# Kernel tuning notes

Measured on AMD Instinct MI355X. Metric: run time of the kernel, lower is better.

## Reference

```python
import jax, jax.numpy as jnp
import numpy as np

C = 17
BETA = 0.95
ALPHA = 5.0
WPC = 3.0  # weight_per_class
IGNORE = 255


def setup_inputs() -> dict:
    key = jax.random.key(0)
    k1, k2 = jax.random.split(key)
    pred = jax.random.normal(k1, (2, C, 200, 200, 16), dtype=jnp.float32)
    ssc_target = jax.random.randint(k2, (2, 200, 200, 16), 0, C, dtype=jnp.int64)
    f1_list = jnp.zeros((C,), dtype=jnp.float32)  # running F1 buffer
    return {"pred": pred, "ssc_target": ssc_target, "f1_list": f1_list}


def _bce_ones(x):
    # F.binary_cross_entropy(x, ones) = -log(x), with torch's log clamp at -100
    return jnp.minimum(-jnp.log(jnp.maximum(x, 1e-38)), 100.0)


def _sem_scal_loss(pred, ssc_target, f1_list):
    B = pred.shape[0]
    ps = jax.nn.softmax(pred, axis=1)                      # [B,C,X,Y,Z]
    mask = (ssc_target != IGNORE)                          # [B,X,Y,Z]
    mf = mask.astype(ps.dtype)
    tgt = jnp.where(mask, ssc_target, 0)                   # safe class index

    # prob of the target class at each voxel -> per-class nominator via segment_sum
    p_at = jnp.take_along_axis(ps, tgt[:, None], axis=1)[:, 0]          # [B,X,Y,Z]
    tgt_flat = tgt.reshape(-1)
    mflat = mf.reshape(-1)
    nominator = jax.ops.segment_sum(p_at.reshape(-1) * mflat, tgt_flat, num_segments=C)
    sum_comp = jax.ops.segment_sum(mflat, tgt_flat, num_segments=C)     # |{target==i}| in mask
    sum_p = jnp.einsum('bcn,bn->c', ps.reshape(B, C, -1), mf.reshape(B, -1))
    n_mask = jnp.sum(mflat)

    has = sum_comp > 0
    precision = jnp.where(sum_p > 0, nominator / jnp.where(sum_p > 0, sum_p, 1.0), 0.0)
    recall = jnp.where(has, nominator / jnp.where(has, sum_comp, 1.0), 0.0)
    neg_comp = n_mask - sum_comp                           # sum(1 - completion_target)
    spec_num = (n_mask - sum_p) - (sum_comp - nominator)   # sum((1-p)*(1-comp))
    specificity = jnp.where(neg_comp > 0, spec_num / jnp.where(neg_comp > 0, neg_comp, 1.0), 0.0)

    loss_list = jnp.where(
        has,
        jnp.where(sum_p > 0, _bce_ones(precision), 0.0)
        + _bce_ones(recall)
        + jnp.where(neg_comp > 0, _bce_ones(specificity), 0.0),
        0.0,
    )

    denom = precision + recall
    f1 = jnp.where(denom > 0, 2.0 * precision * recall / jnp.where(denom > 0, denom, 1.0), 0.0)
    cur_f1 = jnp.where(has, f1, 0.0)
    new_f1 = BETA * f1_list + (1.0 - BETA) * cur_f1        # updated running buffer

    count = jnp.sum(has.astype(ps.dtype))
    weight_pool = WPC * count

    sel = loss_list != 0
    logits = jnp.where(sel, ALPHA * (1.0 - new_f1), -jnp.inf)
    sm = jax.nn.softmax(logits)                            # softmax over selected classes
    weighted = loss_list * (1.0 + weight_pool * sm)
    loss = jnp.sum(weighted) / (count * (1.0 + WPC))
    return loss


def reference(pred, ssc_target, f1_list):
    return _sem_scal_loss(pred, ssc_target, f1_list)
```

## Files before the change

kernel.cpp:

```cpp
#include <hip/hip_runtime.h>
#include <math.h>

#define NC 17
#define PLANE 640000
#define H2 (PLANE / 2)
#define J 5
#define BPB 250
#define NBLK1 (2 * BPB)
#define PCOLS 504
#define BETA_C 0.95f
#define ALPHA_C 5.0f
#define WPC_C 3.0f
#define IGNORE_C 255

#define DPP_ADD(v, ctrl)                                                        \
    do {                                                                        \
        int _t = __builtin_amdgcn_update_dpp(0, __float_as_int(v), (ctrl),      \
                                             0xf, 0xf, true);                   \
        (v) += __int_as_float(_t);                                              \
    } while (0)

__device__ __forceinline__ float wave_sum_dpp(float v) {
    DPP_ADD(v, 0x111);
    DPP_ADD(v, 0x112);
    DPP_ADD(v, 0x114);
    DPP_ADD(v, 0x118);
    DPP_ADD(v, 0x142);
    DPP_ADD(v, 0x143);
    return v;
}


__global__ __launch_bounds__(256) void al_reduce1(const float* __restrict__ pred,
                                                  const int* __restrict__ tgt,
                                                  float* __restrict__ part) {
    const int bb  = blockIdx.x;
    const int b   = (bb >= BPB) ? 1 : 0;
    const int base = (bb - b * BPB) * (256 * J);
    const int tid = (int)threadIdx.x;
    const float2* p0 = reinterpret_cast<const float2*>(pred) + (size_t)(b * NC) * H2;
    const int2*   tg = reinterpret_cast<const int2*>(tgt) + (size_t)b * H2;

    __shared__ float lds[3 * NC];
    if (tid < 3 * NC) lds[tid] = 0.f;

    float sump[NC];
#pragma unroll
    for (int c = 0; c < NC; ++c) sump[c] = 0.f;

    float2 xA[NC], xB[NC];
    int2 tA, tB;

#define LOAD_SLAB(X, T, s)                                                      \
    do {                                                                        \
        const int n2 = base + (s) * 256 + tid;                                  \
        _Pragma("unroll")                                                       \
        for (int c = 0; c < NC; ++c) X[c] = p0[(size_t)c * H2 + n2];            \
        T = tg[n2];                                                             \
    } while (0)

#define COMP_SLAB(X, T)                                                         \
    do {                                                                        \
        float2 ss = make_float2(0.f, 0.f);                                      \
        _Pragma("unroll")                                                       \
        for (int c = 0; c < NC; ++c) {                                          \
            X[c].x = __expf(X[c].x); ss.x += X[c].x;                            \
            X[c].y = __expf(X[c].y); ss.y += X[c].y;                            \
        }                                                                       \
        const float j0 = (T.x != IGNORE_C) ? __builtin_amdgcn_rcpf(ss.x) : 0.f; \
        const float j1 = (T.y != IGNORE_C) ? __builtin_amdgcn_rcpf(ss.y) : 0.f; \
        float e0 = 0.f, e1 = 0.f;                                               \
        _Pragma("unroll")                                                       \
        for (int c = 0; c < NC; ++c) {                                          \
            sump[c] += X[c].x * j0 + X[c].y * j1;                               \
            e0 = (c == T.x) ? X[c].x : e0;                                      \
            e1 = (c == T.y) ? X[c].y : e1;                                      \
        }                                                                       \
        if (T.x != IGNORE_C) { atomicAdd(&lds[T.x], e0 * j0);                   \
                               atomicAdd(&lds[2 * NC + T.x], 1.0f); }           \
        if (T.y != IGNORE_C) { atomicAdd(&lds[T.y], e1 * j1);                   \
                               atomicAdd(&lds[2 * NC + T.y], 1.0f); }           \
    } while (0)

    LOAD_SLAB(xA, tA, 0);
    LOAD_SLAB(xB, tB, 1);
    __syncthreads();

    COMP_SLAB(xA, tA);
    LOAD_SLAB(xA, tA, 2);
    COMP_SLAB(xB, tB);
    LOAD_SLAB(xB, tB, 3);
    COMP_SLAB(xA, tA);
    LOAD_SLAB(xA, tA, 4);
    COMP_SLAB(xB, tB);
    COMP_SLAB(xA, tA);

#undef LOAD_SLAB
#undef COMP_SLAB

#pragma unroll
    for (int c = 0; c < NC; ++c) sump[c] = wave_sum_dpp(sump[c]);
    if ((tid & 63) == 63) {
#pragma unroll
        for (int c = 0; c < NC; ++c) atomicAdd(&lds[NC + c], sump[c]);
    }
    __syncthreads();

    if (tid < 3 * NC)
        part[(size_t)tid * PCOLS + bb] = lds[tid];
}

__global__ __launch_bounds__(256) void al_reduce2(const float* __restrict__ part,
                                                  float* __restrict__ acc) {
    const int r = blockIdx.x;
    const int tid = (int)threadIdx.x;
    const float* p = part + (size_t)r * PCOLS;

    float s = 0.f;
#pragma unroll
    for (int k = 0; k < 2; ++k) {
        const int i = tid + k * 256;
        s += (i < NBLK1) ? p[i] : 0.f;
    }
    s = wave_sum_dpp(s);

    __shared__ float w[4];
    if ((tid & 63) == 63) w[tid >> 6] = s;
    __syncthreads();
    if (tid == 0) acc[r] = (w[0] + w[1]) + (w[2] + w[3]);
}

__device__ __forceinline__ float bce_ones(float x) {
    return fminf(-logf(fmaxf(x, 1e-38f)), 100.0f);
}

__global__ void al_finalize(const float* __restrict__ acc,
                            const float* __restrict__ f1_list,
                            float* __restrict__ out) {
    if (threadIdx.x != 0 || blockIdx.x != 0) return;

    float nom[NC], sump[NC], cnt[NC];
    float n_mask = 0.f;
    for (int c = 0; c < NC; ++c) {
        nom[c]  = acc[c];
        sump[c] = acc[NC + c];
        cnt[c]  = acc[2 * NC + c];
        n_mask += cnt[c];
    }

    float loss_list[NC], newf1[NC];
    float count = 0.f;
    for (int c = 0; c < NC; ++c) {
        const bool has = cnt[c] > 0.f;
        const float prec = (sump[c] > 0.f) ? nom[c] / sump[c] : 0.f;
        const float rec  = has ? nom[c] / cnt[c] : 0.f;
        const float negc = n_mask - cnt[c];
        const float spec_num = (n_mask - sump[c]) - (cnt[c] - nom[c]);
        const float spec = (negc > 0.f) ? spec_num / negc : 0.f;

        float ll = 0.f;
        if (has) {
            ll  = (sump[c] > 0.f) ? bce_ones(prec) : 0.f;
            ll += bce_ones(rec);
            ll += (negc > 0.f) ? bce_ones(spec) : 0.f;
        }
        loss_list[c] = ll;

        const float den = prec + rec;
        const float f1  = (den > 0.f) ? 2.f * prec * rec / den : 0.f;
        const float cur = has ? f1 : 0.f;
        newf1[c] = BETA_C * f1_list[c] + (1.f - BETA_C) * cur;
        count += has ? 1.f : 0.f;
    }

    const float wp = WPC_C * count;

    float mxl = -INFINITY;
    for (int c = 0; c < NC; ++c) {
        const float lg = (loss_list[c] != 0.f) ? ALPHA_C * (1.f - newf1[c]) : -INFINITY;
        mxl = fmaxf(mxl, lg);
    }
    float e[NC];
    float se = 0.f;
    for (int c = 0; c < NC; ++c) {
        const float lg = (loss_list[c] != 0.f) ? ALPHA_C * (1.f - newf1[c]) : -INFINITY;
        e[c] = expf(lg - mxl);
        se += e[c];
    }

    float total = 0.f;
    for (int c = 0; c < NC; ++c) {
        const float sm = e[c] / se;
        total += loss_list[c] * (1.f + wp * sm);
    }
    out[0] = total / (count * (1.f + WPC_C));
}

extern "C" void kernel_launch(void* const* d_in, const int* in_sizes, int n_in,
                              void* d_out, int out_size, void* d_ws, size_t ws_size,
                              hipStream_t stream) {
    const float* pred    = (const float*)d_in[0];
    const int*   tgt     = (const int*)d_in[1];
    const float* f1_list = (const float*)d_in[2];
    float* out  = (float*)d_out;
    float* part = (float*)d_ws;
    float* acc  = part + (size_t)(3 * NC) * PCOLS;

    al_reduce1<<<dim3(NBLK1), dim3(256), 0, stream>>>(pred, tgt, part);
    al_reduce2<<<dim3(3 * NC), dim3(256), 0, stream>>>(part, acc);
    al_finalize<<<dim3(1), dim3(64), 0, stream>>>(acc, f1_list, out);
}
```

Measured before the change: 36.01 us.

## Fuse reduction and finalize into one kernel with last-block-done pattern

Replaces the three-kernel pipeline (per-block partial write, cross-block reduce, single-thread finalize) with one kernel. Each block atomically adds its per-class sums into padded global accumulators, and the last block to increment a done counter computes the final loss. This removes two kernel launches and the partials buffer, at the cost of a memset, global float atomics, and reliance on ordering between other waves' atomics and the counter increment (there is no block barrier before the counter). Summation order also becomes nondeterministic.

Measured after the change: 46.64 us. 29.5% more time.

```diff
diff --git a/kernel.cpp b/kernel.cpp
--- a/kernel.cpp
+++ b/kernel.cpp
@@ -7,7 +7,8 @@
 #define J 5
 #define BPB 250
 #define NBLK1 (2 * BPB)
-#define PCOLS 504
+#define SLOT 16
+#define DONE_IDX (3 * NC * SLOT)
 #define BETA_C 0.95f
 #define ALPHA_C 5.0f
 #define WPC_C 3.0f
@@ -30,10 +31,17 @@
     return v;
 }
 
+__device__ __forceinline__ float bce_ones(float x) {
+    return fminf(-logf(fmaxf(x, 1e-38f)), 100.0f);
+}
 
-__global__ __launch_bounds__(256) void al_reduce1(const float* __restrict__ pred,
-                                                  const int* __restrict__ tgt,
-                                                  float* __restrict__ part) {
+
+__global__ __launch_bounds__(256) void al_fused(const float* __restrict__ pred,
+                                                const int* __restrict__ tgt,
+                                                const float* __restrict__ f1_list,
+                                                float* __restrict__ acc,
+                                                unsigned* __restrict__ done,
+                                                float* __restrict__ out) {
     const int bb  = blockIdx.x;
     const int b   = (bb >= BPB) ? 1 : 0;
     const int base = (bb - b * BPB) * (256 * J);
@@ -106,45 +114,21 @@
     }
     __syncthreads();
 
-    if (tid < 3 * NC)
-        part[(size_t)tid * PCOLS + bb] = lds[tid];
-}
+    if (tid < 3 * NC) atomicAdd(&acc[tid * SLOT], lds[tid]);
 
-__global__ __launch_bounds__(256) void al_reduce2(const float* __restrict__ part,
-                                                  float* __restrict__ acc) {
-    const int r = blockIdx.x;
-    const int tid = (int)threadIdx.x;
-    const float* p = part + (size_t)r * PCOLS;
+    if (tid != 0) return;
 
-    float s = 0.f;
+    asm volatile("s_waitcnt vmcnt(0)" ::: "memory");
+    const unsigned old = atomicAdd(done, 1u);
+    if (old != (unsigned)(NBLK1 - 1)) return;
+
+    float nom[NC], sump2[NC], cnt[NC];
+    float n_mask = 0.f;
 #pragma unroll
-    for (int k = 0; k < 2; ++k) {
-        const int i = tid + k * 256;
-        s += (i < NBLK1) ? p[i] : 0.f;
-    }
-    s = wave_sum_dpp(s);
-
-    __shared__ float w[4];
-    if ((tid & 63) == 63) w[tid >> 6] = s;
-    __syncthreads();
-    if (tid == 0) acc[r] = (w[0] + w[1]) + (w[2] + w[3]);
-}
-
-__device__ __forceinline__ float bce_ones(float x) {
-    return fminf(-logf(fmaxf(x, 1e-38f)), 100.0f);
-}
-
-__global__ void al_finalize(const float* __restrict__ acc,
-                            const float* __restrict__ f1_list,
-                            float* __restrict__ out) {
-    if (threadIdx.x != 0 || blockIdx.x != 0) return;
-
-    float nom[NC], sump[NC], cnt[NC];
-    float n_mask = 0.f;
     for (int c = 0; c < NC; ++c) {
-        nom[c]  = acc[c];
-        sump[c] = acc[NC + c];
-        cnt[c]  = acc[2 * NC + c];
+        nom[c]   = __hip_atomic_load(&acc[c * SLOT],            __ATOMIC_RELAXED, __HIP_MEMORY_SCOPE_AGENT);
+        sump2[c] = __hip_atomic_load(&acc[(NC + c) * SLOT],     __ATOMIC_RELAXED, __HIP_MEMORY_SCOPE_AGENT);
+        cnt[c]   = __hip_atomic_load(&acc[(2 * NC + c) * SLOT], __ATOMIC_RELAXED, __HIP_MEMORY_SCOPE_AGENT);
         n_mask += cnt[c];
     }
 
@@ -152,15 +136,15 @@
     float count = 0.f;
     for (int c = 0; c < NC; ++c) {
         const bool has = cnt[c] > 0.f;
-        const float prec = (sump[c] > 0.f) ? nom[c] / sump[c] : 0.f;
+        const float prec = (sump2[c] > 0.f) ? nom[c] / sump2[c] : 0.f;
         const float rec  = has ? nom[c] / cnt[c] : 0.f;
         const float negc = n_mask - cnt[c];
-        const float spec_num = (n_mask - sump[c]) - (cnt[c] - nom[c]);
+        const float spec_num = (n_mask - sump2[c]) - (cnt[c] - nom[c]);
         const float spec = (negc > 0.f) ? spec_num / negc : 0.f;
 
         float ll = 0.f;
         if (has) {
-            ll  = (sump[c] > 0.f) ? bce_ones(prec) : 0.f;
+            ll  = (sump2[c] > 0.f) ? bce_ones(prec) : 0.f;
             ll += bce_ones(rec);
             ll += (negc > 0.f) ? bce_ones(spec) : 0.f;
         }
@@ -203,10 +187,9 @@
     const int*   tgt     = (const int*)d_in[1];
     const float* f1_list = (const float*)d_in[2];
     float* out  = (float*)d_out;
-    float* part = (float*)d_ws;
-    float* acc  = part + (size_t)(3 * NC) * PCOLS;
+    float* acc  = (float*)d_ws;
+    unsigned* done = (unsigned*)d_ws + DONE_IDX;
 
-    al_reduce1<<<dim3(NBLK1), dim3(256), 0, stream>>>(pred, tgt, part);
-    al_reduce2<<<dim3(3 * NC), dim3(256), 0, stream>>>(part, acc);
-    al_finalize<<<dim3(1), dim3(64), 0, stream>>>(acc, f1_list, out);
+    hipMemsetAsync(d_ws, 0, (DONE_IDX + 16) * sizeof(float), stream);
+    al_fused<<<dim3(NBLK1), dim3(256), 0, stream>>>(pred, tgt, f1_list, acc, done, out);
 }
```
